# Kernel tuning notes

Hardware: AMD Instinct MI355X
Metric: run time of the kernel (lower is better)

The kernel has to match this reference:

```python
import jax, jax.numpy as jnp
import numpy as np

AUX_LOSS_ALPHA = 0.01
TOP_K = 2
N_EXPERTS = 64


def setup_inputs() -> dict:
    key = jax.random.key(0)
    k1, k2 = jax.random.split(key)
    B, S, H, E = 4, 4096, 2048, N_EXPERTS
    hidden_states = jax.random.normal(k1, (B, S, H), dtype=jnp.float32)
    # kaiming_uniform_(a=sqrt(5)) ~ U(-1/sqrt(H), 1/sqrt(H))
    bound = 1.0 / np.sqrt(H)
    weight = jax.random.uniform(k2, (E, H), dtype=jnp.float32, minval=-bound, maxval=bound)
    return {"hidden_states": hidden_states, "weight": weight}


def reference(hidden_states, weight):
    B, S, H = hidden_states.shape
    E, K = N_EXPERTS, TOP_K
    x = hidden_states.reshape(-1, H)              # [T, H], T = B*S
    logits = jnp.einsum('th,eh->te', x, weight)   # router GEMM [T, E]
    scores = jax.nn.softmax(logits, axis=-1)
    topk_weight, topk_idx = jax.lax.top_k(scores, K)  # [T, K]
    # norm_topk_prob (K > 1)
    topk_weight = topk_weight / (jnp.sum(topk_weight, axis=-1, keepdims=True) + 1e-20)
    # seq_aux auxiliary loss (training path)
    idx2d = topk_idx.reshape(B, S * K)            # [B, S*K]
    ce = jnp.zeros((B, E), dtype=scores.dtype)
    ce = ce.at[jnp.arange(B)[:, None], idx2d].add(1.0)
    ce = ce / (S * K / E)
    scores3 = scores.reshape(B, S, E)
    aux_loss = jnp.mean(jnp.sum(ce * jnp.mean(scores3, axis=1), axis=1)) * AUX_LOSS_ALPHA
    return topk_idx, topk_weight, aux_loss
```

## Files before the change

### kernel.cpp

```cpp
#include <hip/hip_runtime.h>
#include <math.h>


#define TT 16384
#define HH 2048
#define EE 64
#define BB 4
#define M_TOK 16
#define TAU 2e-3f
#define NREP 8
#define NBLK (TT / M_TOK)

typedef float v4f __attribute__((ext_vector_type(4)));
typedef float f4v __attribute__((ext_vector_type(4)));
typedef short s8v __attribute__((ext_vector_type(8)));

__device__ __forceinline__ unsigned short f2bf(float f) {
    unsigned u = __float_as_uint(f);
    return (unsigned short)((u + 0x7fffu + ((u >> 16) & 1u)) >> 16);
}
__device__ __forceinline__ float bf2f(unsigned short h) {
    return __uint_as_float(((unsigned)h) << 16);
}

__global__ void prep_b(const float* __restrict__ w,
                       unsigned short* __restrict__ bhi,
                       unsigned short* __restrict__ blo,
                       float* __restrict__ zreg) {
    if (blockIdx.x == 0) {
        for (int i = threadIdx.x; i < 2 * NREP * BB * EE; i += 256) zreg[i] = 0.f;
    }
    int idx = blockIdx.x * blockDim.x + threadIdx.x;
    int j    = idx & 7;
    int lane = (idx >> 3) & 63;
    int ks   = (idx >> 9) & 63;
    int nt   = idx >> 15;
    int e = nt * 16 + (lane & 15);
    int k = ks * 32 + (lane >> 4) * 8 + j;
    float f = w[e * HH + k];
    unsigned short h = f2bf(f);
    bhi[idx] = h;
    blo[idx] = f2bf(f - bf2f(h));
}

__global__ __launch_bounds__(256, 4) void gemm_gate(
    const float* __restrict__ x,
    const unsigned short* __restrict__ bhi, const unsigned short* __restrict__ blo,
    const float* __restrict__ w,
    float* __restrict__ out_idx, float* __restrict__ out_w,
    float* __restrict__ g_cnt, float* __restrict__ g_ssum) {

    __shared__ float accLDS[3][16][64];
    __shared__ float lg[M_TOK][68];
    __shared__ float bssum[EE];
    __shared__ float bcnt[EE];
    __shared__ int   fl[M_TOK];
    __shared__ int   fl_cnt;

    const int tid  = threadIdx.x;
    const int wave = tid >> 6;
    const int lane = tid & 63;
    const int tok0 = blockIdx.x * M_TOK;

    if (tid < EE) { bssum[tid] = 0.f; bcnt[tid] = 0.f; }
    if (tid == 0) fl_cnt = 0;

    const float* __restrict__ xp =
        x + (size_t)(tok0 + (lane & 15)) * HH + wave * 512 + (lane >> 4) * 8;
    const unsigned short* __restrict__ bhp = bhi + ((size_t)(wave * 16) * 64 + lane) * 8;
    const unsigned short* __restrict__ blp = blo + ((size_t)(wave * 16) * 64 + lane) * 8;

    f4v acc[4];
#pragma unroll
    for (int nt = 0; nt < 4; ++nt) acc[nt] = f4v{0.f, 0.f, 0.f, 0.f};

#pragma unroll
    for (int ks = 0; ks < 16; ++ks) {
        v4f xa = *(const v4f*)(xp + ks * 32);
        v4f xb = *(const v4f*)(xp + ks * 32 + 4);
        s8v bhv[4], blv[4];
#pragma unroll
        for (int nt = 0; nt < 4; ++nt) {
            bhv[nt] = *(const s8v*)(bhp + (size_t)nt * 32768 + ks * 512);
            blv[nt] = *(const s8v*)(blp + (size_t)nt * 32768 + ks * 512);
        }
        s8v ah, al;
#pragma unroll
        for (int j = 0; j < 8; ++j) {
            float f = (j < 4) ? xa[j] : xb[j - 4];
            unsigned short h = f2bf(f);
            ah[j] = (short)h;
            al[j] = (short)f2bf(f - bf2f(h));
        }
#pragma unroll
        for (int nt = 0; nt < 4; ++nt) {
            acc[nt] = __builtin_amdgcn_mfma_f32_16x16x32_bf16(ah, bhv[nt], acc[nt], 0, 0, 0);
            acc[nt] = __builtin_amdgcn_mfma_f32_16x16x32_bf16(ah, blv[nt], acc[nt], 0, 0, 0);
            acc[nt] = __builtin_amdgcn_mfma_f32_16x16x32_bf16(al, bhv[nt], acc[nt], 0, 0, 0);
        }
    }

    if (wave != 0) {
#pragma unroll
        for (int nt = 0; nt < 4; ++nt)
#pragma unroll
            for (int r = 0; r < 4; ++r)
                accLDS[wave - 1][nt * 4 + r][lane] = acc[nt][r];
    }
    __syncthreads();
    if (wave == 0) {
#pragma unroll
        for (int nt = 0; nt < 4; ++nt)
#pragma unroll
            for (int r = 0; r < 4; ++r) {
                float s = acc[nt][r] + accLDS[0][nt * 4 + r][lane]
                        + accLDS[1][nt * 4 + r][lane] + accLDS[2][nt * 4 + r][lane];
                lg[(lane >> 4) * 4 + r][nt * 16 + (lane & 15)] = s;
            }
    }
    __syncthreads();

    float ssum_l = 0.f;

#pragma unroll
    for (int r = 0; r < 4; ++r) {
        const int tl = wave * 4 + r;
        const int t  = tok0 + tl;
        float l = lg[tl][lane];

        float mx = l;
#pragma unroll
        for (int off = 32; off; off >>= 1) mx = fmaxf(mx, __shfl_xor(mx, off, 64));
        float p = __expf(l - mx);
        float Z = p;
#pragma unroll
        for (int off = 32; off; off >>= 1) Z += __shfl_xor(Z, off, 64);
        ssum_l += p / Z;

        float v = l;
        int cand[3]; float cl[3];
#pragma unroll
        for (int q = 0; q < 3; ++q) {
            float bv = v; int bi = lane;
#pragma unroll
            for (int off = 32; off; off >>= 1) {
                float ov = __shfl_xor(bv, off, 64);
                int   oi = __shfl_xor(bi, off, 64);
                if (ov > bv || (ov == bv && oi < bi)) { bv = ov; bi = oi; }
            }
            cand[q] = bi; cl[q] = bv;
            if (lane == bi) v = -3.4e38f;
        }

        if (lane == 0) {
            atomicAdd(&bcnt[cand[0]], 1.f);
            atomicAdd(&bcnt[cand[1]], 1.f);
            float w1 = 1.f / (1.f + __expf(cl[1] - cl[0]));
            out_idx[t * 2]     = (float)cand[0];
            out_idx[t * 2 + 1] = (float)cand[1];
            out_w[t * 2]       = w1;
            out_w[t * 2 + 1]   = 1.f - w1;
            if (cl[0] - cl[1] < TAU || cl[1] - cl[2] < TAU) {
                int pos = atomicAdd(&fl_cnt, 1);
                fl[pos] = tl;
            }
        }
    }

    atomicAdd(&bssum[lane], ssum_l);
    __syncthreads();

    {
        const int b   = tok0 >> 12;
        const int rep = (blockIdx.x & (NREP - 1)) * (BB * EE);
        if (tid < EE)
            atomicAdd(&g_cnt[rep + b * EE + tid], bcnt[tid]);
        else if (tid < 2 * EE)
            atomicAdd(&g_ssum[rep + b * EE + (tid - EE)], bssum[tid - EE]);
    }

    const int nfl = fl_cnt;
    for (int i = wave; i < nfl; i += 4) {
        const int tl = fl[i];
        const int t  = tok0 + tl;
        float l = lg[tl][lane];

        float v = l;
        int cand4[4];
#pragma unroll
        for (int q = 0; q < 4; ++q) {
            float bv = v; int bi = lane;
#pragma unroll
            for (int off = 32; off; off >>= 1) {
                float ov = __shfl_xor(bv, off, 64);
                int   oi = __shfl_xor(bi, off, 64);
                if (ov > bv || (ov == bv && oi < bi)) { bv = ov; bi = oi; }
            }
            cand4[q] = bi;
            if (lane == bi) v = -3.4e38f;
        }

        const float* __restrict__ xt  = x + (size_t)t * HH;
        const float* __restrict__ w0p = w + (size_t)cand4[0] * HH;
        const float* __restrict__ w1p = w + (size_t)cand4[1] * HH;
        const float* __restrict__ w2p = w + (size_t)cand4[2] * HH;
        const float* __restrict__ w3p = w + (size_t)cand4[3] * HH;
        double d0 = 0.0, d1 = 0.0, d2 = 0.0, d3 = 0.0;
#pragma unroll
        for (int ii = 0; ii < 8; ++ii) {
            const int k = ii * 256 + lane * 4;
            v4f xv = *(const v4f*)(xt + k);
            v4f a0 = *(const v4f*)(w0p + k);
            v4f a1 = *(const v4f*)(w1p + k);
            v4f a2 = *(const v4f*)(w2p + k);
            v4f a3 = *(const v4f*)(w3p + k);
            double dx0 = (double)xv.x, dx1 = (double)xv.y;
            double dx2 = (double)xv.z, dx3 = (double)xv.w;
            d0 = fma(dx0, (double)a0.x, d0); d0 = fma(dx1, (double)a0.y, d0);
            d0 = fma(dx2, (double)a0.z, d0); d0 = fma(dx3, (double)a0.w, d0);
            d1 = fma(dx0, (double)a1.x, d1); d1 = fma(dx1, (double)a1.y, d1);
            d1 = fma(dx2, (double)a1.z, d1); d1 = fma(dx3, (double)a1.w, d1);
            d2 = fma(dx0, (double)a2.x, d2); d2 = fma(dx1, (double)a2.y, d2);
            d2 = fma(dx2, (double)a2.z, d2); d2 = fma(dx3, (double)a2.w, d2);
            d3 = fma(dx0, (double)a3.x, d3); d3 = fma(dx1, (double)a3.y, d3);
            d3 = fma(dx2, (double)a3.z, d3); d3 = fma(dx3, (double)a3.w, d3);
        }
#pragma unroll
        for (int off = 32; off; off >>= 1) {
            d0 += __shfl_xor(d0, off, 64);
            d1 += __shfl_xor(d1, off, 64);
            d2 += __shfl_xor(d2, off, 64);
            d3 += __shfl_xor(d3, off, 64);
        }

        double bd[4] = {d0, d1, d2, d3};
        int e1 = cand4[0]; double l1 = bd[0];
#pragma unroll
        for (int q = 1; q < 4; ++q)
            if (bd[q] > l1 || (bd[q] == l1 && cand4[q] < e1)) { l1 = bd[q]; e1 = cand4[q]; }
        int e2 = -1; double l2 = -1e300;
#pragma unroll
        for (int q = 0; q < 4; ++q) {
            if (cand4[q] == e1) continue;
            if (e2 < 0 || bd[q] > l2 || (bd[q] == l2 && cand4[q] < e2)) { l2 = bd[q]; e2 = cand4[q]; }
        }

        double w1d = 1.0 / (1.0 + exp(l2 - l1));
        if (lane == 0) {
            out_idx[t * 2]     = (float)e1;
            out_idx[t * 2 + 1] = (float)e2;
            out_w[t * 2]       = (float)w1d;
            out_w[t * 2 + 1]   = (float)(1.0 - w1d);
        }
    }
}

__global__ void finalize(const float* __restrict__ g_cnt,
                         const float* __restrict__ g_ssum,
                         float* __restrict__ aux_out) {
    int lane = threadIdx.x;
    float a = 0.f;
    for (int b = 0; b < BB; ++b) {
        float c = 0.f, ss = 0.f;
#pragma unroll
        for (int r = 0; r < NREP; ++r) {
            c  += g_cnt[r * (BB * EE) + b * EE + lane];
            ss += g_ssum[r * (BB * EE) + b * EE + lane];
        }
        a += c * ss;
    }
#pragma unroll
    for (int off = 32; off; off >>= 1) a += __shfl_xor(a, off, 64);
    if (lane == 0) aux_out[0] = a * (0.01f / (4.f * 128.f * 4096.f));
}

extern "C" void kernel_launch(void* const* d_in, const int* in_sizes, int n_in,
                              void* d_out, int out_size, void* d_ws, size_t ws_size,
                              hipStream_t stream) {
    const float* x = (const float*)d_in[0];
    const float* w = (const float*)d_in[1];
    float* out = (float*)d_out;
    float* out_idx = out;
    float* out_w   = out + 2 * TT;
    float* aux     = out + 4 * TT;

    unsigned short* bhi = (unsigned short*)d_ws;
    unsigned short* blo = bhi + (size_t)EE * HH;
    float* g_cnt  = (float*)(blo + (size_t)EE * HH);
    float* g_ssum = g_cnt + NREP * BB * EE;

    prep_b<<<(EE * HH) / 256, 256, 0, stream>>>(w, bhi, blo, g_cnt);
    gemm_gate<<<NBLK, 256, 0, stream>>>(x, bhi, blo, w, out_idx, out_w,
                                        g_cnt, g_ssum);
    finalize<<<1, 64, 0, stream>>>(g_cnt, g_ssum, aux);
}
```

Baseline: 230.8 us.

## Double tile to 32 tokens with 8 waves and register double-buffered loads

```diff
diff --git a/kernel.cpp b/kernel.cpp
--- a/kernel.cpp
+++ b/kernel.cpp
@@ -6,7 +6,7 @@
 #define HH 2048
 #define EE 64
 #define BB 4
-#define M_TOK 16
+#define M_TOK 32
 #define TAU 2e-3f
 #define NREP 8
 #define NBLK (TT / M_TOK)
@@ -43,88 +43,123 @@
     blo[idx] = f2bf(f - bf2f(h));
 }
 
-__global__ __launch_bounds__(256, 4) void gemm_gate(
+__global__ __launch_bounds__(512, 4) void gemm_gate(
     const float* __restrict__ x,
     const unsigned short* __restrict__ bhi, const unsigned short* __restrict__ blo,
     const float* __restrict__ w,
     float* __restrict__ out_idx, float* __restrict__ out_w,
     float* __restrict__ g_cnt, float* __restrict__ g_ssum) {
 
-    __shared__ float accLDS[3][16][64];
+    __shared__ float accLDS[3][M_TOK][64];
     __shared__ float lg[M_TOK][68];
     __shared__ float bssum[EE];
     __shared__ float bcnt[EE];
     __shared__ int   fl[M_TOK];
     __shared__ int   fl_cnt;
 
-    const int tid  = threadIdx.x;
-    const int wave = tid >> 6;
-    const int lane = tid & 63;
-    const int tok0 = blockIdx.x * M_TOK;
+    const int tid   = threadIdx.x;
+    const int wavei = tid >> 6;
+    const int lane  = tid & 63;
+    const int kq    = wavei >> 1;
+    const int nth   = wavei & 1;
+    const int tok0  = blockIdx.x * M_TOK;
 
     if (tid < EE) { bssum[tid] = 0.f; bcnt[tid] = 0.f; }
     if (tid == 0) fl_cnt = 0;
 
-    const float* __restrict__ xp =
-        x + (size_t)(tok0 + (lane & 15)) * HH + wave * 512 + (lane >> 4) * 8;
-    const unsigned short* __restrict__ bhp = bhi + ((size_t)(wave * 16) * 64 + lane) * 8;
-    const unsigned short* __restrict__ blp = blo + ((size_t)(wave * 16) * 64 + lane) * 8;
-
-    f4v acc[4];
-#pragma unroll
-    for (int nt = 0; nt < 4; ++nt) acc[nt] = f4v{0.f, 0.f, 0.f, 0.f};
+    const float* __restrict__ xp0 =
+        x + (size_t)(tok0 + (lane & 15)) * HH + kq * 512 + (lane >> 4) * 8;
+    const float* __restrict__ xp1 = xp0 + (size_t)16 * HH;
+    const unsigned short* __restrict__ bhp =
+        bhi + ((size_t)((nth * 2) * 64 + kq * 16) * 64 + lane) * 8;
+    const unsigned short* __restrict__ blp =
+        blo + ((size_t)((nth * 2) * 64 + kq * 16) * 64 + lane) * 8;
+
+    f4v acc00 = {0.f,0.f,0.f,0.f}, acc01 = {0.f,0.f,0.f,0.f};
+    f4v acc10 = {0.f,0.f,0.f,0.f}, acc11 = {0.f,0.f,0.f,0.f};
+
+    v4f A[2][4];
+    s8v BH[2][2], BL[2][2];
+
+    A[0][0] = *(const v4f*)(xp0);
+    A[0][1] = *(const v4f*)(xp0 + 4);
+    A[0][2] = *(const v4f*)(xp1);
+    A[0][3] = *(const v4f*)(xp1 + 4);
+    BH[0][0] = *(const s8v*)(bhp);
+    BH[0][1] = *(const s8v*)(bhp + 32768);
+    BL[0][0] = *(const s8v*)(blp);
+    BL[0][1] = *(const s8v*)(blp + 32768);
 
 #pragma unroll
     for (int ks = 0; ks < 16; ++ks) {
-        v4f xa = *(const v4f*)(xp + ks * 32);
-        v4f xb = *(const v4f*)(xp + ks * 32 + 4);
-        s8v bhv[4], blv[4];
-#pragma unroll
-        for (int nt = 0; nt < 4; ++nt) {
-            bhv[nt] = *(const s8v*)(bhp + (size_t)nt * 32768 + ks * 512);
-            blv[nt] = *(const s8v*)(blp + (size_t)nt * 32768 + ks * 512);
-        }
-        s8v ah, al;
+        const int cur = ks & 1, nxt = cur ^ 1;
+        if (ks < 15) {
+            A[nxt][0] = *(const v4f*)(xp0 + (ks + 1) * 32);
+            A[nxt][1] = *(const v4f*)(xp0 + (ks + 1) * 32 + 4);
+            A[nxt][2] = *(const v4f*)(xp1 + (ks + 1) * 32);
+            A[nxt][3] = *(const v4f*)(xp1 + (ks + 1) * 32 + 4);
+            BH[nxt][0] = *(const s8v*)(bhp + (ks + 1) * 512);
+            BH[nxt][1] = *(const s8v*)(bhp + 32768 + (ks + 1) * 512);
+            BL[nxt][0] = *(const s8v*)(blp + (ks + 1) * 512);
+            BL[nxt][1] = *(const s8v*)(blp + 32768 + (ks + 1) * 512);
+        }
+        s8v ah0, al0, ah1, al1;
 #pragma unroll
         for (int j = 0; j < 8; ++j) {
-            float f = (j < 4) ? xa[j] : xb[j - 4];
-            unsigned short h = f2bf(f);
-            ah[j] = (short)h;
-            al[j] = (short)f2bf(f - bf2f(h));
-        }
-#pragma unroll
-        for (int nt = 0; nt < 4; ++nt) {
-            acc[nt] = __builtin_amdgcn_mfma_f32_16x16x32_bf16(ah, bhv[nt], acc[nt], 0, 0, 0);
-            acc[nt] = __builtin_amdgcn_mfma_f32_16x16x32_bf16(ah, blv[nt], acc[nt], 0, 0, 0);
-            acc[nt] = __builtin_amdgcn_mfma_f32_16x16x32_bf16(al, bhv[nt], acc[nt], 0, 0, 0);
-        }
-    }
-
-    if (wave != 0) {
-#pragma unroll
-        for (int nt = 0; nt < 4; ++nt)
-#pragma unroll
-            for (int r = 0; r < 4; ++r)
-                accLDS[wave - 1][nt * 4 + r][lane] = acc[nt][r];
-    }
-    __syncthreads();
-    if (wave == 0) {
-#pragma unroll
-        for (int nt = 0; nt < 4; ++nt)
+            float f0 = (j < 4) ? A[cur][0][j] : A[cur][1][j - 4];
+            float f1 = (j < 4) ? A[cur][2][j] : A[cur][3][j - 4];
+            unsigned short h0 = f2bf(f0), h1 = f2bf(f1);
+            ah0[j] = (short)h0; al0[j] = (short)f2bf(f0 - bf2f(h0));
+            ah1[j] = (short)h1; al1[j] = (short)f2bf(f1 - bf2f(h1));
+        }
+        acc00 = __builtin_amdgcn_mfma_f32_16x16x32_bf16(ah0, BH[cur][0], acc00, 0, 0, 0);
+        acc00 = __builtin_amdgcn_mfma_f32_16x16x32_bf16(ah0, BL[cur][0], acc00, 0, 0, 0);
+        acc00 = __builtin_amdgcn_mfma_f32_16x16x32_bf16(al0, BH[cur][0], acc00, 0, 0, 0);
+        acc01 = __builtin_amdgcn_mfma_f32_16x16x32_bf16(ah0, BH[cur][1], acc01, 0, 0, 0);
+        acc01 = __builtin_amdgcn_mfma_f32_16x16x32_bf16(ah0, BL[cur][1], acc01, 0, 0, 0);
+        acc01 = __builtin_amdgcn_mfma_f32_16x16x32_bf16(al0, BH[cur][1], acc01, 0, 0, 0);
+        acc10 = __builtin_amdgcn_mfma_f32_16x16x32_bf16(ah1, BH[cur][0], acc10, 0, 0, 0);
+        acc10 = __builtin_amdgcn_mfma_f32_16x16x32_bf16(ah1, BL[cur][0], acc10, 0, 0, 0);
+        acc10 = __builtin_amdgcn_mfma_f32_16x16x32_bf16(al1, BH[cur][0], acc10, 0, 0, 0);
+        acc11 = __builtin_amdgcn_mfma_f32_16x16x32_bf16(ah1, BH[cur][1], acc11, 0, 0, 0);
+        acc11 = __builtin_amdgcn_mfma_f32_16x16x32_bf16(ah1, BL[cur][1], acc11, 0, 0, 0);
+        acc11 = __builtin_amdgcn_mfma_f32_16x16x32_bf16(al1, BH[cur][1], acc11, 0, 0, 0);
+    }
+
+    {
+        const int r0 = (lane >> 4) * 4;
+        const int c0 = nth * 32 + (lane & 15);
+        if (kq != 0) {
 #pragma unroll
             for (int r = 0; r < 4; ++r) {
-                float s = acc[nt][r] + accLDS[0][nt * 4 + r][lane]
-                        + accLDS[1][nt * 4 + r][lane] + accLDS[2][nt * 4 + r][lane];
-                lg[(lane >> 4) * 4 + r][nt * 16 + (lane & 15)] = s;
-            }
-    }
-    __syncthreads();
+                accLDS[kq - 1][r0 + r][c0]           = acc00[r];
+                accLDS[kq - 1][r0 + r][c0 + 16]      = acc01[r];
+                accLDS[kq - 1][16 + r0 + r][c0]      = acc10[r];
+                accLDS[kq - 1][16 + r0 + r][c0 + 16] = acc11[r];
+            }
+        }
+        __syncthreads();
+        if (kq == 0) {
+#pragma unroll
+            for (int r = 0; r < 4; ++r) {
+                lg[r0 + r][c0] = acc00[r] + accLDS[0][r0 + r][c0]
+                               + accLDS[1][r0 + r][c0] + accLDS[2][r0 + r][c0];
+                lg[r0 + r][c0 + 16] = acc01[r] + accLDS[0][r0 + r][c0 + 16]
+                               + accLDS[1][r0 + r][c0 + 16] + accLDS[2][r0 + r][c0 + 16];
+                lg[16 + r0 + r][c0] = acc10[r] + accLDS[0][16 + r0 + r][c0]
+                               + accLDS[1][16 + r0 + r][c0] + accLDS[2][16 + r0 + r][c0];
+                lg[16 + r0 + r][c0 + 16] = acc11[r] + accLDS[0][16 + r0 + r][c0 + 16]
+                               + accLDS[1][16 + r0 + r][c0 + 16] + accLDS[2][16 + r0 + r][c0 + 16];
+            }
+        }
+        __syncthreads();
+    }
 
     float ssum_l = 0.f;
 
 #pragma unroll
     for (int r = 0; r < 4; ++r) {
-        const int tl = wave * 4 + r;
+        const int tl = wavei * 4 + r;
         const int t  = tok0 + tl;
         float l = lg[tl][lane];
 
@@ -180,7 +215,7 @@
     }
 
     const int nfl = fl_cnt;
-    for (int i = wave; i < nfl; i += 4) {
+    for (int i = wavei; i < nfl; i += 8) {
         const int tl = fl[i];
         const int t  = tok0 + tl;
         float l = lg[tl][lane];
@@ -290,7 +325,7 @@
     float* g_ssum = g_cnt + NREP * BB * EE;
 
     prep_b<<<(EE * HH) / 256, 256, 0, stream>>>(w, bhi, blo, g_cnt);
-    gemm_gate<<<NBLK, 256, 0, stream>>>(x, bhi, blo, w, out_idx, out_w,
+    gemm_gate<<<NBLK, 512, 0, stream>>>(x, bhi, blo, w, out_idx, out_w,
                                         g_cnt, g_ssum);
     finalize<<<1, 64, 0, stream>>>(g_cnt, g_ssum, aux);
 }
```

New measurement: 223.5 us. 1.03x faster.

## Split router GEMM K across eight waves with LDS atomic reduction and cheaper bf16 split

Applied to the files above, without the earlier changes.

```diff
diff --git a/kernel.cpp b/kernel.cpp
--- a/kernel.cpp
+++ b/kernel.cpp
@@ -14,6 +14,7 @@
 typedef float v4f __attribute__((ext_vector_type(4)));
 typedef float f4v __attribute__((ext_vector_type(4)));
 typedef short s8v __attribute__((ext_vector_type(8)));
+typedef int   i4v __attribute__((ext_vector_type(4)));
 
 __device__ __forceinline__ unsigned short f2bf(float f) {
     unsigned u = __float_as_uint(f);
@@ -21,6 +22,18 @@
 }
 __device__ __forceinline__ float bf2f(unsigned short h) {
     return __uint_as_float(((unsigned)h) << 16);
+}
+
+__device__ __forceinline__ void cvt2(float f0, float f1, unsigned& hi, unsigned& lo) {
+    unsigned u0 = __float_as_uint(f0), u1 = __float_as_uint(f1);
+    hi = (u0 >> 16) | (u1 & 0xffff0000u);
+    float l0 = f0 - __uint_as_float(u0 & 0xffff0000u);
+    float l1 = f1 - __uint_as_float(u1 & 0xffff0000u);
+    lo = (__float_as_uint(l0) >> 16) | (__float_as_uint(l1) & 0xffff0000u);
+}
+__device__ __forceinline__ s8v pack4(unsigned a, unsigned b, unsigned c, unsigned d) {
+    i4v t = {(int)a, (int)b, (int)c, (int)d};
+    return __builtin_bit_cast(s8v, t);
 }
 
 __global__ void prep_b(const float* __restrict__ w,
@@ -43,39 +56,39 @@
     blo[idx] = f2bf(f - bf2f(h));
 }
 
-__global__ __launch_bounds__(256, 4) void gemm_gate(
+__global__ __launch_bounds__(512, 8) void gemm_gate(
     const float* __restrict__ x,
     const unsigned short* __restrict__ bhi, const unsigned short* __restrict__ blo,
     const float* __restrict__ w,
     float* __restrict__ out_idx, float* __restrict__ out_w,
     float* __restrict__ g_cnt, float* __restrict__ g_ssum) {
 
-    __shared__ float accLDS[3][16][64];
     __shared__ float lg[M_TOK][68];
     __shared__ float bssum[EE];
     __shared__ float bcnt[EE];
     __shared__ int   fl[M_TOK];
     __shared__ int   fl_cnt;
 
-    const int tid  = threadIdx.x;
-    const int wave = tid >> 6;
-    const int lane = tid & 63;
-    const int tok0 = blockIdx.x * M_TOK;
-
+    const int tid   = threadIdx.x;
+    const int wavei = tid >> 6;
+    const int lane  = tid & 63;
+    const int tok0  = blockIdx.x * M_TOK;
+
+    for (int i = tid; i < M_TOK * 68; i += 512) (&lg[0][0])[i] = 0.f;
     if (tid < EE) { bssum[tid] = 0.f; bcnt[tid] = 0.f; }
     if (tid == 0) fl_cnt = 0;
 
     const float* __restrict__ xp =
-        x + (size_t)(tok0 + (lane & 15)) * HH + wave * 512 + (lane >> 4) * 8;
-    const unsigned short* __restrict__ bhp = bhi + ((size_t)(wave * 16) * 64 + lane) * 8;
-    const unsigned short* __restrict__ blp = blo + ((size_t)(wave * 16) * 64 + lane) * 8;
+        x + (size_t)(tok0 + (lane & 15)) * HH + wavei * 256 + (lane >> 4) * 8;
+    const unsigned short* __restrict__ bhp = bhi + ((size_t)(wavei * 8) * 64 + lane) * 8;
+    const unsigned short* __restrict__ blp = blo + ((size_t)(wavei * 8) * 64 + lane) * 8;
 
     f4v acc[4];
 #pragma unroll
     for (int nt = 0; nt < 4; ++nt) acc[nt] = f4v{0.f, 0.f, 0.f, 0.f};
 
 #pragma unroll
-    for (int ks = 0; ks < 16; ++ks) {
+    for (int ks = 0; ks < 8; ++ks) {
         v4f xa = *(const v4f*)(xp + ks * 32);
         v4f xb = *(const v4f*)(xp + ks * 32 + 4);
         s8v bhv[4], blv[4];
@@ -84,14 +97,13 @@
             bhv[nt] = *(const s8v*)(bhp + (size_t)nt * 32768 + ks * 512);
             blv[nt] = *(const s8v*)(blp + (size_t)nt * 32768 + ks * 512);
         }
-        s8v ah, al;
-#pragma unroll
-        for (int j = 0; j < 8; ++j) {
-            float f = (j < 4) ? xa[j] : xb[j - 4];
-            unsigned short h = f2bf(f);
-            ah[j] = (short)h;
-            al[j] = (short)f2bf(f - bf2f(h));
-        }
+        unsigned h01, l01, h23, l23, h45, l45, h67, l67;
+        cvt2(xa.x, xa.y, h01, l01);
+        cvt2(xa.z, xa.w, h23, l23);
+        cvt2(xb.x, xb.y, h45, l45);
+        cvt2(xb.z, xb.w, h67, l67);
+        s8v ah = pack4(h01, h23, h45, h67);
+        s8v al = pack4(l01, l23, l45, l67);
 #pragma unroll
         for (int nt = 0; nt < 4; ++nt) {
             acc[nt] = __builtin_amdgcn_mfma_f32_16x16x32_bf16(ah, bhv[nt], acc[nt], 0, 0, 0);
@@ -100,31 +112,24 @@
         }
     }
 
-    if (wave != 0) {
+    __syncthreads();
+
+    {
+        const int r0 = (lane >> 4) * 4;
+        const int c  = lane & 15;
 #pragma unroll
         for (int nt = 0; nt < 4; ++nt)
 #pragma unroll
             for (int r = 0; r < 4; ++r)
-                accLDS[wave - 1][nt * 4 + r][lane] = acc[nt][r];
+                atomicAdd(&lg[r0 + r][nt * 16 + c], acc[nt][r]);
     }
     __syncthreads();
-    if (wave == 0) {
-#pragma unroll
-        for (int nt = 0; nt < 4; ++nt)
-#pragma unroll
-            for (int r = 0; r < 4; ++r) {
-                float s = acc[nt][r] + accLDS[0][nt * 4 + r][lane]
-                        + accLDS[1][nt * 4 + r][lane] + accLDS[2][nt * 4 + r][lane];
-                lg[(lane >> 4) * 4 + r][nt * 16 + (lane & 15)] = s;
-            }
-    }
-    __syncthreads();
 
     float ssum_l = 0.f;
 
 #pragma unroll
-    for (int r = 0; r < 4; ++r) {
-        const int tl = wave * 4 + r;
+    for (int r = 0; r < 2; ++r) {
+        const int tl = wavei * 2 + r;
         const int t  = tok0 + tl;
         float l = lg[tl][lane];
 
@@ -180,7 +185,7 @@
     }
 
     const int nfl = fl_cnt;
-    for (int i = wave; i < nfl; i += 4) {
+    for (int i = wavei; i < nfl; i += 8) {
         const int tl = fl[i];
         const int t  = tok0 + tl;
         float l = lg[tl][lane];
@@ -290,7 +295,7 @@
     float* g_ssum = g_cnt + NREP * BB * EE;
 
     prep_b<<<(EE * HH) / 256, 256, 0, stream>>>(w, bhi, blo, g_cnt);
-    gemm_gate<<<NBLK, 256, 0, stream>>>(x, bhi, blo, w, out_idx, out_w,
+    gemm_gate<<<NBLK, 512, 0, stream>>>(x, bhi, blo, w, out_idx, out_w,
                                         g_cnt, g_ssum);
     finalize<<<1, 64, 0, stream>>>(g_cnt, g_ssum, aux);
 }
```

Result: slower. 295.0 us (+27.8%).
